# Performance work log

Hardware: AMD Instinct MI355X
Metric: run time of the kernel (lower is better)

The kernel has to match this reference:

```python
import jax, jax.numpy as jnp
import numpy as np

B, L, D, NH, NITEMS = 256, 200, 128, 2, 100000
HD = D // NH
LAMB = 0.6
NEG = -1e9

_PARAM_SHAPES = dict(
    item_emb=(NITEMS, D), pos_emb=(L, D),
    W_ei=(D, D), b_ei=(D,), W_eo=(D, D), b_eo=(D,), b_iah=(D,), b_oah=(D,),
    w_ih=(3 * D, 2 * D), b_ih=(3 * D,), w_hh=(3 * D, D), b_hh=(3 * D,),
    ln1_g=(D,), ln1_b=(D,),
    Wq=(D, D), bq=(D,), Wk=(D, D), bk=(D,), Wv=(D, D), bv=(D,), Wo=(D, D), bo=(D,),
    ln2_g=(D,), ln2_b=(D,), W1=(D, D), b1=(D,), W2=(D, D), b2=(D,),
    lnf_g=(D,), lnf_b=(D,),
)


def setup_inputs() -> dict:
    key = jax.random.key(0)
    ks = jax.random.split(key, len(_PARAM_SHAPES) + 2)
    stdv = 1.0 / np.sqrt(D)  # GCSAN._init_weights: uniform(-stdv, stdv) on ALL params
    p = {}
    for i, (name, shp) in enumerate(_PARAM_SHAPES.items()):
        p[name] = jax.random.uniform(ks[i], shp, jnp.float32, -stdv, stdv)
    lens = jax.random.randint(ks[-2], (B,), L // 4, L + 1)
    vals = jax.random.randint(ks[-1], (B, L), 1, NITEMS)
    # trailing zero padding, as the original break-on-zero loop assumes
    seqs = jnp.where(jnp.arange(L)[None, :] < lens[:, None], vals, 0).astype(jnp.int32)
    p['seqs'] = seqs
    p['lens'] = lens.astype(jnp.int32)
    return p


def _ln(x, g, b):
    mu = x.mean(-1, keepdims=True)
    var = ((x - mu) ** 2).mean(-1, keepdims=True)
    return (x - mu) / jnp.sqrt(var + 1e-5) * g + b


def _build_graph(seqs):
    # Vectorized replacement of _get_slice (per-row np.unique + adjacency build)
    def per_row(seq):
        s = jnp.sort(seq)
        first = jnp.concatenate([jnp.ones((1,), bool), s[1:] != s[:-1]])
        pos = jnp.cumsum(first) - 1  # compaction target of each first-occurrence
        items = jnp.zeros((L,), seq.dtype).at[jnp.where(first, pos, L)].set(s, mode='drop')
        n_u = first.sum()
        search = jnp.where(jnp.arange(L) < n_u, items, jnp.iinfo(jnp.int32).max)
        alias = jnp.searchsorted(search, seq).astype(jnp.int32)
        return items, alias
    items, alias = jax.vmap(per_row)(seqs)
    valid = seqs[:, 1:] > 0  # edge (i -> i+1) exists until first pad
    u = jnp.where(valid, alias[:, :-1], L)  # route masked edges to dummy row L
    v = jnp.where(valid, alias[:, 1:], L)
    bidx = jnp.arange(B)[:, None]
    uA = jnp.zeros((B, L + 1, L + 1), jnp.float32).at[bidx, u, v].set(1.0)[:, :L, :L]
    in_deg = jnp.maximum(uA.sum(1), 1.0)
    out_deg = jnp.maximum(uA.sum(2), 1.0)
    A_in = jnp.swapaxes(uA, 1, 2) / in_deg[:, :, None]   # A[i,j] = uA[j,i]/in_deg[i]
    A_out = uA / out_deg[:, :, None]                     # A[i,k] = uA[i,k]/out_deg[i]
    return alias, jnp.concatenate([A_in, A_out], axis=2), items  # A: [B, L, 2L]


def reference(item_emb, pos_emb, W_ei, b_ei, W_eo, b_eo, b_iah, b_oah,
              w_ih, b_ih, w_hh, b_hh, ln1_g, ln1_b, Wq, bq, Wk, bk, Wv, bv,
              Wo, bo, ln2_g, ln2_b, W1, b1, W2, b2, lnf_g, lnf_b, seqs, lens):
    alias, A, items = _build_graph(seqs)
    hidden = item_emb[items]  # [B, L, D]
    # SR-GNN gated cell, step = n_layers = 1
    for _ in range(1):
        h_in = jnp.einsum('bij,bjd->bid', A[:, :, :L], hidden @ W_ei.T + b_ei) + b_iah
        h_out = jnp.einsum('bij,bjd->bid', A[:, :, L:], hidden @ W_eo.T + b_eo) + b_oah
        gi = jnp.concatenate([h_in, h_out], -1) @ w_ih.T + b_ih
        gh = hidden @ w_hh.T + b_hh
        i_r, i_i, i_n = jnp.split(gi, 3, -1)
        h_r, h_i, h_n = jnp.split(gh, 3, -1)
        r = jax.nn.sigmoid(i_r + h_r)
        z = jax.nn.sigmoid(i_i + h_i)
        ng = jnp.tanh(i_n + r * h_n)
        hidden = ng + z * (hidden - ng)
    bidx = jnp.arange(B)
    seq_hidden = hidden[bidx[:, None], alias]  # alias-gather back to sequence order
    last_idx = lens - 1
    ht = seq_hidden[bidx, last_idx]
    x = seq_hidden + pos_emb[None, :, :]
    tl_mask = (seqs > 0)[:, :, None].astype(x.dtype)
    x = x * tl_mask
    causal = jnp.triu(jnp.ones((L, L), bool), 1)  # True = masked future (bidirectional=False)
    # SASRec-style block: ln -> MHA residual -> ln -> pointwise FFN residual
    q_in = _ln(x, ln1_g, ln1_b)
    heads = lambda t: t.reshape(B, L, NH, HD).transpose(0, 2, 1, 3)
    q = heads(q_in @ Wq.T + bq)
    k = heads(x @ Wk.T + bk)
    v = heads(x @ Wv.T + bv)
    sc = jnp.einsum('bhqd,bhkd->bhqk', q, k) / jnp.sqrt(jnp.asarray(HD, x.dtype))
    sc = jnp.where(causal[None, None], NEG, sc)
    attn = jax.nn.softmax(sc, -1)
    mo = jnp.einsum('bhqk,bhkd->bhqd', attn, v).transpose(0, 2, 1, 3).reshape(B, L, D) @ Wo.T + bo
    x = q_in + mo
    h = _ln(x, ln2_g, ln2_b)
    x = h + jax.nn.relu(h @ W1.T + b1) @ W2.T + b2
    x = x * tl_mask
    log_feats = _ln(x, lnf_g, lnf_b)
    out = log_feats[bidx, last_idx]
    return LAMB * out + (1.0 - LAMB) * ht
```

## Files before the change

kernel.cpp:

```cpp
#include <hip/hip_runtime.h>
#include <hip/hip_bf16.h>

#define Bb 256
#define Ll 200
#define Dd 128
#define BL (Bb*Ll)

typedef __hip_bfloat16 bf16;
typedef __attribute__((ext_vector_type(8))) short short8;
typedef __attribute__((ext_vector_type(4))) unsigned short ushort4v;
typedef __attribute__((ext_vector_type(4))) float floatx4;

__device__ __forceinline__ float b2f(bf16 v) { return __bfloat162float(v); }
__device__ __forceinline__ bf16  f2b(float v) { return __float2bfloat16(v); }
__device__ __forceinline__ float us2f(unsigned short u) { return __uint_as_float(((unsigned)u) << 16); }
__device__ __forceinline__ unsigned short f2us(float v) { bf16 t = f2b(v); return *(unsigned short*)&t; }
__device__ __forceinline__ float ldf(const void* p, int i, int f32) {
  return f32 ? ((const float*)p)[i] : b2f(((const bf16*)p)[i]);
}
__device__ __forceinline__ int detect_f32(const unsigned short* __restrict__ w) {
  unsigned short u = w[threadIdx.x & 63];
  return (__ballot(((u >> 7) & 0xFF) >= 0x7F) != 0ull) ? 1 : 0;
}
__device__ __forceinline__ void load_lds16(const void* g, void* l) {
  __builtin_amdgcn_global_load_lds((const __attribute__((address_space(1))) unsigned int*)g,
                                   (__attribute__((address_space(3))) unsigned int*)l, 16, 0, 0);
}

struct PackP {
  const void *W_ei,*W_eo,*w_ih,*w_hh,*Wk,*Wv,*Wqp,*Wop,*W1p,*W2p,*pos;
  const void *b_ei,*b_eo,*b_ih,*b_hh,*bk,*bv,*bqp,*bop,*b1p,*b2p,*biah,*boah;
  const void *ln1g,*ln1b,*ln2g,*ln2b,*lnfg,*lnfb;
  bf16 *cWhe,*cWih,*cWhh,*cWkv,*cWq,*cWo,*cW1,*cW2,*cPos;
  float *bias_he,*bias_gi,*bias_gh,*bias_kv,*cbq,*cbo,*cb1,*cb2,*cbiah,*cboah,*cln;
};
__global__ __launch_bounds__(256) void k0_pack(PackP p) {
  int idx = blockIdx.x * 256 + threadIdx.x;
  int f32 = detect_f32((const unsigned short*)p.W_ei);
  if (idx < 131072) {
    if (idx < 32768) {
      int r = idx >> 7, c = idx & 127;
      p.cWhe[idx] = f2b(r < 128 ? ldf(p.W_ei, r*128+c, f32) : ldf(p.W_eo, (r-128)*128+c, f32));
    } else p.cWih[idx-32768] = f2b(ldf(p.w_ih, idx-32768, f32));
  } else if (idx < 278528) {
    if (idx < 180224)      p.cWhh[idx-131072] = f2b(ldf(p.w_hh, idx-131072, f32));
    else if (idx < 212992) {
      int i = idx - 180224; int r = i >> 7, c = i & 127;
      p.cWkv[i] = f2b(r < 128 ? ldf(p.Wk, r*128+c, f32) : ldf(p.Wv, (r-128)*128+c, f32));
    }
    else if (idx < 229376) p.cWq[idx-212992] = f2b(ldf(p.Wqp, idx-212992, f32));
    else if (idx < 245760) p.cWo[idx-229376] = f2b(ldf(p.Wop, idx-229376, f32));
    else if (idx < 262144) p.cW1[idx-245760] = f2b(ldf(p.W1p, idx-245760, f32));
    else                   p.cW2[idx-262144] = f2b(ldf(p.W2p, idx-262144, f32));
  } else if (idx < 304128) {
    p.cPos[idx-278528] = f2b(ldf(p.pos, idx-278528, f32));
  } else {
    int j = idx - 304128;
    if      (j < 256)  p.bias_he[j]     = (j<128) ? ldf(p.b_ei,j,f32) : ldf(p.b_eo,j-128,f32);
    else if (j < 640)  p.bias_gi[j-256] = ldf(p.b_ih, j-256, f32);
    else if (j < 1024) p.bias_gh[j-640] = ldf(p.b_hh, j-640, f32);
    else if (j < 1280) { int c=j-1024; p.bias_kv[c] = (c<128)? ldf(p.bk,c,f32): ldf(p.bv,c-128,f32); }
    else if (j < 1408) p.cbq[j-1280]   = ldf(p.bqp, j-1280, f32);
    else if (j < 1536) p.cbo[j-1408]   = ldf(p.bop, j-1408, f32);
    else if (j < 1664) p.cb1[j-1536]   = ldf(p.b1p, j-1536, f32);
    else if (j < 1792) p.cb2[j-1664]   = ldf(p.b2p, j-1664, f32);
    else if (j < 1920) p.cbiah[j-1792] = ldf(p.biah, j-1792, f32);
    else if (j < 2048) p.cboah[j-1920] = ldf(p.boah, j-1920, f32);
    else {
      int i = j - 2048, g = i >> 7, c2 = i & 127;
      const void* s6 = g==0?p.ln1g: g==1?p.ln1b: g==2?p.ln2g: g==3?p.ln2b: g==4?p.lnfg: p.lnfb;
      p.cln[i] = ldf(s6, c2, f32);
    }
  }
}

__global__ __launch_bounds__(256) void k1_graph(const int* __restrict__ seqs,
    int* __restrict__ alias_g, int* __restrict__ items_g,
    float* __restrict__ rin_g, float* __restrict__ rout_g,
    unsigned* __restrict__ adj_g, unsigned* __restrict__ adjT_g)
{
  __shared__ int s[Ll], al[Ll], its[Ll];
  __shared__ unsigned char isf[Ll];
  __shared__ unsigned adjL[Ll*8], adjTL[Ll*8];
  int b = blockIdx.x, t = threadIdx.x;
  if (t < Ll) s[t] = seqs[b*Ll + t];
  for (int i = t; i < Ll*8; i += 256) { adjL[i] = 0u; adjTL[i] = 0u; }
  __syncthreads();
  if (t < Ll) {
    int v = s[t]; bool f = true;
    for (int j = 0; j < t; j++) if (s[j] == v) { f = false; break; }
    isf[t] = f ? 1 : 0; its[t] = 0;
  }
  __syncthreads();
  if (t < Ll) {
    int v = s[t], r = 0;
    for (int j = 0; j < Ll; j++) r += (isf[j] && s[j] < v);
    al[t] = r;
  }
  __syncthreads();
  if (t < Ll && isf[t]) its[al[t]] = s[t];
  if (t < Ll-1 && s[t+1] > 0) {
    int u = al[t], v = al[t+1];
    atomicOr(&adjL [u*8 + (v >> 5)], 1u << (v & 31));
    atomicOr(&adjTL[v*8 + (u >> 5)], 1u << (u & 31));
  }
  __syncthreads();
  if (t < Ll) {
    int od = 0, id = 0;
    for (int wd = 0; wd < 7; wd++) { od += __popc(adjL[t*8+wd]); id += __popc(adjTL[t*8+wd]); }
    rout_g [b*Ll + t] = 1.0f / (float)max(od, 1);
    rin_g  [b*Ll + t] = 1.0f / (float)max(id, 1);
    alias_g[b*Ll + t] = al[t];
    items_g[b*Ll + t] = its[t];
  }
  for (int i = t; i < Ll*8; i += 256) { adj_g[b*Ll*8 + i] = adjL[i]; adjT_g[b*Ll*8 + i] = adjTL[i]; }
}

__global__ __launch_bounds__(256) void k2_gather(const void* __restrict__ emb, const void* __restrict__ wei,
    const int* __restrict__ items_g, bf16* __restrict__ hidden)
{
  int idx = blockIdx.x * 256 + threadIdx.x;
  int f32 = detect_f32((const unsigned short*)wei);
  int n = idx >> 4, jv = idx & 15;
  int it = items_g[n];
  short8 o;
  if (f32) {
    const float* e = (const float*)emb + (size_t)it * 128 + jv * 8;
#pragma unroll
    for (int j = 0; j < 8; j++) o[j] = (short)f2us(e[j]);
  } else {
    o = ((const short8*)((const bf16*)emb + (size_t)it * 128))[jv];
  }
  ((short8*)hidden)[idx] = o;
}

template<int K>
__global__ __launch_bounds__(256) void gemm5(const bf16* __restrict__ A, const bf16* __restrict__ W,
    const float* __restrict__ bias,
    bf16* __restrict__ out_lo, int Nlo, bf16* __restrict__ out_hi, int Nhi, int split)
{
  __shared__ short As[128*64];
  __shared__ short Ws[128*64];
  int t = threadIdx.x;
  int wave = t >> 6, lane = t & 63;
  int q = lane >> 4, mr = lane & 15;
  int wm = wave & 1, wn = wave >> 1;
  int m0 = blockIdx.x * 128, n0 = blockIdx.y * 128;
  int lr = lane >> 3, slot = lane & 7;
  int gch = slot ^ lr;
  floatx4 acc[4][4] = {};
  for (int k0 = 0; k0 < K; k0 += 64) {
#pragma unroll
    for (int i = 0; i < 4; i++) {
      int c = wave*4 + i;
      int r = c*8 + lr;
      load_lds16(A + (size_t)(m0 + r) * K + k0 + gch*8, &As[c*512]);
      load_lds16(W + (size_t)(n0 + r) * K + k0 + gch*8, &Ws[c*512]);
    }
    __syncthreads();
#pragma unroll
    for (int kk = 0; kk < 2; kk++) {
      short8 af[4], wf[4];
#pragma unroll
      for (int i = 0; i < 4; i++) {
        int row = wm*64 + i*16 + mr;
        af[i] = *(const short8*)(&As[row*64 + ((kk*4+q) ^ (mr&7))*8]);
      }
#pragma unroll
      for (int j = 0; j < 4; j++) {
        int row = wn*64 + j*16 + mr;
        wf[j] = *(const short8*)(&Ws[row*64 + ((kk*4+q) ^ (mr&7))*8]);
      }
#pragma unroll
      for (int i = 0; i < 4; i++)
#pragma unroll
        for (int j = 0; j < 4; j++)
          acc[i][j] = __builtin_amdgcn_mfma_f32_16x16x32_bf16(wf[j], af[i], acc[i][j], 0, 0, 0);
    }
    __syncthreads();
  }
#pragma unroll
  for (int j = 0; j < 4; j++) {
    int ng = n0 + wn*64 + j*16 + q*4;
    floatx4 bs = *(const floatx4*)(bias + ng);
    bf16* outp; int col, stride;
    if (ng < split) { outp = out_lo; col = ng; stride = Nlo; }
    else            { outp = out_hi; col = ng - split; stride = Nhi; }
#pragma unroll
    for (int i = 0; i < 4; i++) {
      int m = m0 + wm*64 + i*16 + mr;
      ushort4v o;
#pragma unroll
      for (int e = 0; e < 4; e++) o[e] = f2us(acc[i][j][e] + bs[e]);
      *(ushort4v*)(outp + (size_t)m * stride + col) = o;
    }
  }
}

__global__ __launch_bounds__(256) void k3_agg(const bf16* __restrict__ he,
    const unsigned* __restrict__ adj_g, const unsigned* __restrict__ adjT_g,
    const float* __restrict__ rin_g, const float* __restrict__ rout_g,
    const float* __restrict__ cbiah, const float* __restrict__ cboah, bf16* __restrict__ hio)
{
  int b = blockIdx.x / 25, chunk = blockIdx.x % 25;
  int wave = threadIdx.x >> 6, lane = threadIdx.x & 63;
  bool isIn = lane < 32;
  int c = isIn ? 4*lane : 128 + 4*(lane-32);
  const bf16* heb = he + (size_t)b * Ll * 256;
  bf16* hiob = hio + (size_t)b * Ll * 256;
  float bias0 = isIn ? cbiah[c]   : cboah[c-128];
  float bias1 = isIn ? cbiah[c+1] : cboah[c-127];
  float bias2 = isIn ? cbiah[c+2] : cboah[c-126];
  float bias3 = isIn ? cbiah[c+3] : cboah[c-125];
#pragma unroll
  for (int s = 0; s < 2; s++) {
    int i = chunk*8 + wave + 4*s;
    const unsigned* mrow = (isIn ? adjT_g : adj_g) + ((size_t)b*Ll + i) * 8;
    float a0=0.f, a1=0.f, a2=0.f, a3=0.f;
    for (int wd = 0; wd < 7; wd++) {
      unsigned bits = mrow[wd];
      while (bits) {
        int j = (wd << 5) + __builtin_ctz(bits); bits &= bits - 1;
        ushort4v h4 = *(const ushort4v*)(heb + (size_t)j*256 + c);
        a0 += us2f(h4.x); a1 += us2f(h4.y); a2 += us2f(h4.z); a3 += us2f(h4.w);
      }
    }
    float r = isIn ? rin_g[b*Ll + i] : rout_g[b*Ll + i];
    ushort4v o;
    o.x = f2us(bias0 + r*a0); o.y = f2us(bias1 + r*a1);
    o.z = f2us(bias2 + r*a2); o.w = f2us(bias3 + r*a3);
    *(ushort4v*)(hiob + (size_t)i*256 + c) = o;
  }
}

__global__ __launch_bounds__(256) void k4_gru(const bf16* __restrict__ gi, const bf16* __restrict__ gh,
                                              bf16* __restrict__ hidden)
{
  int idx = blockIdx.x * 256 + threadIdx.x;
  int n = idx >> 4, jv = idx & 15;
  const short8* gin = (const short8*)(gi + (size_t)n * 384);
  const short8* ghn = (const short8*)(gh + (size_t)n * 384);
  short8 vir = gin[jv], vii = gin[16+jv], vnn = gin[32+jv];
  short8 whr = ghn[jv], whi = ghn[16+jv], whn = ghn[32+jv];
  short8 hv  = ((const short8*)hidden)[idx];
  short8 o;
#pragma unroll
  for (int e = 0; e < 8; e++) {
    float ir = us2f((unsigned short)vir[e]), ii = us2f((unsigned short)vii[e]), inn = us2f((unsigned short)vnn[e]);
    float hr = us2f((unsigned short)whr[e]), hi = us2f((unsigned short)whi[e]), hn = us2f((unsigned short)whn[e]);
    float r  = 1.f / (1.f + __expf(-(ir + hr)));
    float z  = 1.f / (1.f + __expf(-(ii + hi)));
    float arg = inn + r * hn;
    float ex = __expf(-2.f * arg);
    float ng = (1.f - ex) / (1.f + ex);
    float h  = us2f((unsigned short)hv[e]);
    o[e] = (short)f2us(ng + z * (h - ng));
  }
  ((short8*)hidden)[idx] = o;
}

__global__ __launch_bounds__(256) void k5_x(const bf16* __restrict__ hidden, const int* __restrict__ alias_g,
    const int* __restrict__ seqs, const int* __restrict__ lens,
    const bf16* __restrict__ cPos, bf16* __restrict__ x, float* __restrict__ ht)
{
  int idx = blockIdx.x * 256 + threadIdx.x;
  int jv = idx & 15; int bt = idx >> 4; int tpos = bt % Ll; int b = bt / Ll;
  int a = alias_g[bt];
  short8 hv = ((const short8*)(hidden + ((size_t)b*Ll + a) * Dd))[jv];
  short8 pv = ((const short8*)(cPos + tpos * Dd))[jv];
  bool valid = seqs[bt] > 0;
  bool isLast = (tpos == lens[b] - 1);
  short8 o;
#pragma unroll
  for (int e = 0; e < 8; e++) {
    float sh = us2f((unsigned short)hv[e]);
    float val = valid ? sh + us2f((unsigned short)pv[e]) : 0.f;
    o[e] = (short)f2us(val);
    if (isLast) ht[b*Dd + jv*8 + e] = sh;
  }
  ((short8*)x)[idx] = o;
}

struct FinalP {
  const bf16 *x, *kv; const float* ht;
  const bf16 *cWq, *cWo, *cW1, *cW2;
  const float *cbq, *cbo, *cb1, *cb2, *cln;
  const int* lens; const void* wei;
  void* out;
};
__device__ float block_sum(float v, float* red) {
  int t = threadIdx.x;
  red[t] = v; __syncthreads();
  for (int s = 128; s > 0; s >>= 1) { if (t < s) red[t] += red[t+s]; __syncthreads(); }
  float r = red[0]; __syncthreads(); return r;
}
__device__ float block_max(float v, float* red) {
  int t = threadIdx.x;
  red[t] = v; __syncthreads();
  for (int s = 128; s > 0; s >>= 1) { if (t < s) red[t] = fmaxf(red[t], red[t+s]); __syncthreads(); }
  float r = red[0]; __syncthreads(); return r;
}
__device__ __forceinline__ float dot128(const bf16* __restrict__ wrow, const float* __restrict__ vin) {
  const short8* wr = (const short8*)wrow;
  float acc = 0.f;
#pragma unroll
  for (int kk = 0; kk < 16; kk++) {
    short8 w8 = wr[kk];
#pragma unroll
    for (int j = 0; j < 8; j++) acc += vin[kk*8 + j] * us2f((unsigned short)w8[j]);
  }
  return acc;
}
__global__ __launch_bounds__(256) void k7_final(FinalP p)
{
  __shared__ float red[256];
  __shared__ float pb[256];
  __shared__ float av4[256];
  __shared__ float qin[128], qv[128], aout[128], hh[128], f1[128];
  int b = blockIdx.x, t = threadIdx.x, c = t;
  int li = p.lens[b] - 1;
  int f32 = detect_f32((const unsigned short*)p.wei);
  float xv = (c < 128) ? b2f(p.x[((size_t)b*Ll + li) * Dd + c]) : 0.f;
  float mu = block_sum((c < 128) ? xv : 0.f, red) * (1.f/128.f);
  float d  = (c < 128) ? xv - mu : 0.f;
  float var = block_sum(d*d, red) * (1.f/128.f);
  float rs = rsqrtf(var + 1e-5f);
  if (c < 128) qin[c] = d * rs * p.cln[c] + p.cln[128+c];
  __syncthreads();
  if (c < 128) qv[c] = p.cbq[c] + dot128(p.cWq + c*128, qin);
  __syncthreads();
  const bf16* kvb = p.kv + (size_t)b * Ll * 256;
  for (int h = 0; h < 2; h++) {
    float sc = -3.0e38f;
    if (t <= li) {
      const short8* kr = (const short8*)(kvb + (size_t)t*256 + h*64);
      float s_ = 0.f;
#pragma unroll
      for (int kk = 0; kk < 8; kk++) {
        short8 k8 = kr[kk];
#pragma unroll
        for (int j = 0; j < 8; j++) s_ += qv[h*64 + kk*8 + j] * us2f((unsigned short)k8[j]);
      }
      sc = s_ * 0.125f;
    }
    float m = block_max(sc, red);
    float e = (t <= li) ? __expf(sc - m) : 0.f;
    pb[t] = e;
    float l = block_sum(e, red);
    int ch = t & 63, part = t >> 6;
    float accv = 0.f;
    for (int j = part; j <= li; j += 4)
      accv += pb[j] * b2f(kvb[(size_t)j*256 + 128 + h*64 + ch]);
    av4[part*64 + ch] = accv;
    __syncthreads();
    if (t < 64) aout[h*64 + t] = (av4[t] + av4[64+t] + av4[128+t] + av4[192+t]) / l;
    __syncthreads();
  }
  float x2v = 0.f;
  if (c < 128) x2v = qin[c] + p.cbo[c] + dot128(p.cWo + c*128, aout);
  mu = block_sum((c < 128) ? x2v : 0.f, red) * (1.f/128.f);
  d  = (c < 128) ? x2v - mu : 0.f;
  var = block_sum(d*d, red) * (1.f/128.f);
  rs = rsqrtf(var + 1e-5f);
  if (c < 128) hh[c] = d * rs * p.cln[256+c] + p.cln[384+c];
  __syncthreads();
  if (c < 128) f1[c] = fmaxf(p.cb1[c] + dot128(p.cW1 + c*128, hh), 0.f);
  __syncthreads();
  float x3v = 0.f;
  if (c < 128) x3v = hh[c] + p.cb2[c] + dot128(p.cW2 + c*128, f1);
  mu = block_sum((c < 128) ? x3v : 0.f, red) * (1.f/128.f);
  d  = (c < 128) ? x3v - mu : 0.f;
  var = block_sum(d*d, red) * (1.f/128.f);
  rs = rsqrtf(var + 1e-5f);
  if (c < 128) {
    float lf = d * rs * p.cln[512+c] + p.cln[640+c];
    float outv = 0.6f * lf + 0.4f * p.ht[b*Dd + c];
    if (f32) ((float*)p.out)[b*Dd + c] = outv;
    else     ((bf16*)p.out)[b*Dd + c]  = f2b(outv);
  }
}

extern "C" void kernel_launch(void* const* d_in, const int* in_sizes, int n_in,
                              void* d_out, int out_size, void* d_ws, size_t ws_size,
                              hipStream_t stream)
{
  (void)in_sizes; (void)n_in; (void)out_size; (void)ws_size;
  const void* item_emb = d_in[0];
  const int* seqs = (const int*)d_in[30];
  const int* lens = (const int*)d_in[31];

  char* wsp = (char*)d_ws;
  size_t o = 0;
  auto alloc = [&](size_t sz) { void* p = wsp + o; o += (sz + 255) & ~(size_t)255; return p; };
  int*      alias_g = (int*)alloc((size_t)BL*4);
  int*      items_g = (int*)alloc((size_t)BL*4);
  float*    rin_g   = (float*)alloc((size_t)BL*4);
  float*    rout_g  = (float*)alloc((size_t)BL*4);
  unsigned* adj_g   = (unsigned*)alloc((size_t)BL*8*4);
  unsigned* adjT_g  = (unsigned*)alloc((size_t)BL*8*4);
  float*    ht_g    = (float*)alloc((size_t)Bb*Dd*4);
  bf16*     cWhe    = (bf16*)alloc(32768*2);
  bf16*     cWhh    = (bf16*)alloc(49152*2);
  bf16*     cWih    = (bf16*)alloc(98304*2);
  bf16*     cWkv    = (bf16*)alloc(32768*2);
  bf16*     cWq     = (bf16*)alloc(16384*2);
  bf16*     cWo     = (bf16*)alloc(16384*2);
  bf16*     cW1     = (bf16*)alloc(16384*2);
  bf16*     cW2     = (bf16*)alloc(16384*2);
  bf16*     cPos    = (bf16*)alloc(25600*2);
  float*    bias_he = (float*)alloc(256*4);
  float*    bias_gh = (float*)alloc(384*4);
  float*    bias_gi = (float*)alloc(384*4);
  float*    bias_kv = (float*)alloc(256*4);
  float*    cbq     = (float*)alloc(128*4);
  float*    cbo     = (float*)alloc(128*4);
  float*    cb1     = (float*)alloc(128*4);
  float*    cb2     = (float*)alloc(128*4);
  float*    cbiah   = (float*)alloc(128*4);
  float*    cboah   = (float*)alloc(128*4);
  float*    cln     = (float*)alloc(768*4);
  bf16*     hidden  = (bf16*)alloc((size_t)BL*128*2);
  bf16*     he      = (bf16*)alloc((size_t)BL*256*2);
  bf16*     hio     = (bf16*)alloc((size_t)BL*256*2);
  bf16*     gi      = (bf16*)alloc((size_t)BL*384*2);
  bf16*     gh      = (bf16*)alloc((size_t)BL*384*2);
  bf16*     x  = he;
  bf16*     kv = hio;

  PackP pp = { d_in[2], d_in[4], d_in[8], d_in[10], d_in[16], d_in[18], d_in[14], d_in[20],
               d_in[24], d_in[26], d_in[1],
               d_in[3], d_in[5], d_in[9], d_in[11], d_in[17], d_in[19], d_in[15], d_in[21],
               d_in[25], d_in[27], d_in[6], d_in[7],
               d_in[12], d_in[13], d_in[22], d_in[23], d_in[28], d_in[29],
               cWhe, cWih, cWhh, cWkv, cWq, cWo, cW1, cW2, cPos,
               bias_he, bias_gi, bias_gh, bias_kv, cbq, cbo, cb1, cb2, cbiah, cboah, cln };
  k0_pack<<<1199, 256, 0, stream>>>(pp);
  k1_graph<<<Bb, 256, 0, stream>>>(seqs, alias_g, items_g, rin_g, rout_g, adj_g, adjT_g);
  k2_gather<<<BL*16/256, 256, 0, stream>>>(item_emb, d_in[2], items_g, hidden);
  gemm5<128><<<dim3(BL/128, 5), 256, 0, stream>>>(hidden, cWhe, bias_he, he, 256, gh, 384, 256);
  k3_agg<<<Bb*25, 256, 0, stream>>>(he, adj_g, adjT_g, rin_g, rout_g, cbiah, cboah, hio);
  gemm5<256><<<dim3(BL/128, 3), 256, 0, stream>>>(hio, cWih, bias_gi, gi, 384, gi, 384, 1<<30);
  k4_gru<<<BL*16/256, 256, 0, stream>>>(gi, gh, hidden);
  k5_x<<<BL*16/256, 256, 0, stream>>>(hidden, alias_g, seqs, lens, cPos, x, ht_g);
  gemm5<128><<<dim3(BL/128, 2), 256, 0, stream>>>(x, cWkv, bias_kv, kv, 256, kv, 256, 1<<30);
  FinalP fp = { x, kv, ht_g, cWq, cWo, cW1, cW2, cbq, cbo, cb1, cb2, cln, lens, d_in[2], d_out };
  k7_final<<<Bb, 256, 0, stream>>>(fp);
}
```

Measured before the change: 321.9 us.

## Use wave-shuffle reductions and process both heads jointly in final kernel

Replaces the shared-memory tree reductions in the final per-sequence kernel with 64-lane shuffle reductions plus a small cross-wave combine. It also computes LayerNorm statistics in a single pass from sum and sum of squares. Both attention heads' scores and softmax are computed together, and the PV accumulation is split into 8 contiguous chunks with 4-wide vector loads. Dot products use four independent accumulators. This removes many __syncthreads barriers and serial dependency chains; single-pass variance is slightly less numerically robust.

```diff
diff --git a/kernel.cpp b/kernel.cpp
--- a/kernel.cpp
+++ b/kernel.cpp
@@ -288,92 +288,133 @@
   const int* lens; const void* wei;
   void* out;
 };
-__device__ float block_sum(float v, float* red) {
-  int t = threadIdx.x;
-  red[t] = v; __syncthreads();
-  for (int s = 128; s > 0; s >>= 1) { if (t < s) red[t] += red[t+s]; __syncthreads(); }
-  float r = red[0]; __syncthreads(); return r;
-}
-__device__ float block_max(float v, float* red) {
-  int t = threadIdx.x;
-  red[t] = v; __syncthreads();
-  for (int s = 128; s > 0; s >>= 1) { if (t < s) red[t] = fmaxf(red[t], red[t+s]); __syncthreads(); }
-  float r = red[0]; __syncthreads(); return r;
-}
-__device__ __forceinline__ float dot128(const bf16* __restrict__ wrow, const float* __restrict__ vin) {
+__device__ __forceinline__ float dot128i(const bf16* __restrict__ wrow, const float* __restrict__ vin) {
   const short8* wr = (const short8*)wrow;
-  float acc = 0.f;
-#pragma unroll
-  for (int kk = 0; kk < 16; kk++) {
-    short8 w8 = wr[kk];
-#pragma unroll
-    for (int j = 0; j < 8; j++) acc += vin[kk*8 + j] * us2f((unsigned short)w8[j]);
-  }
-  return acc;
+  float a0=0.f, a1=0.f, a2=0.f, a3=0.f;
+#pragma unroll
+  for (int kk = 0; kk < 4; kk++) {
+    short8 w0 = wr[kk*4+0], w1 = wr[kk*4+1], w2 = wr[kk*4+2], w3 = wr[kk*4+3];
+#pragma unroll
+    for (int j = 0; j < 8; j++) {
+      a0 += vin[kk*32 +      j] * us2f((unsigned short)w0[j]);
+      a1 += vin[kk*32 + 8  + j] * us2f((unsigned short)w1[j]);
+      a2 += vin[kk*32 + 16 + j] * us2f((unsigned short)w2[j]);
+      a3 += vin[kk*32 + 24 + j] * us2f((unsigned short)w3[j]);
+    }
+  }
+  return (a0+a1)+(a2+a3);
+}
+__device__ __forceinline__ float wave_sum(float v) {
+#pragma unroll
+  for (int m = 1; m < 64; m <<= 1) v += __shfl_xor(v, m, 64);
+  return v;
+}
+__device__ __forceinline__ float wave_max(float v) {
+#pragma unroll
+  for (int m = 1; m < 64; m <<= 1) v = fmaxf(v, __shfl_xor(v, m, 64));
+  return v;
 }
 __global__ __launch_bounds__(256) void k7_final(FinalP p)
 {
-  __shared__ float red[256];
-  __shared__ float pb[256];
-  __shared__ float av4[256];
+  __shared__ float sred[8];
   __shared__ float qin[128], qv[128], aout[128], hh[128], f1[128];
+  __shared__ float pb0[256], pb1[256];
+  __shared__ floatx4 av4[8][32];
   int b = blockIdx.x, t = threadIdx.x, c = t;
+  int w = t >> 6, ln = t & 63;
   int li = p.lens[b] - 1;
   int f32 = detect_f32((const unsigned short*)p.wei);
   float xv = (c < 128) ? b2f(p.x[((size_t)b*Ll + li) * Dd + c]) : 0.f;
-  float mu = block_sum((c < 128) ? xv : 0.f, red) * (1.f/128.f);
-  float d  = (c < 128) ? xv - mu : 0.f;
-  float var = block_sum(d*d, red) * (1.f/128.f);
-  float rs = rsqrtf(var + 1e-5f);
-  if (c < 128) qin[c] = d * rs * p.cln[c] + p.cln[128+c];
-  __syncthreads();
-  if (c < 128) qv[c] = p.cbq[c] + dot128(p.cWq + c*128, qin);
+  float s = wave_sum(xv), s2 = wave_sum(xv*xv);
+  if (ln == 0) { sred[w] = s; sred[4+w] = s2; }
+  __syncthreads();
+  float mu = (sred[0]+sred[1]+sred[2]+sred[3]) * (1.f/128.f);
+  float ms = (sred[4]+sred[5]+sred[6]+sred[7]) * (1.f/128.f);
+  float rs = rsqrtf(fmaxf(ms - mu*mu, 0.f) + 1e-5f);
+  __syncthreads();
+  if (c < 128) qin[c] = (xv - mu) * rs * p.cln[c] + p.cln[128+c];
+  __syncthreads();
+  if (c < 128) qv[c] = p.cbq[c] + dot128i(p.cWq + c*128, qin);
   __syncthreads();
   const bf16* kvb = p.kv + (size_t)b * Ll * 256;
-  for (int h = 0; h < 2; h++) {
-    float sc = -3.0e38f;
-    if (t <= li) {
-      const short8* kr = (const short8*)(kvb + (size_t)t*256 + h*64);
-      float s_ = 0.f;
-#pragma unroll
-      for (int kk = 0; kk < 8; kk++) {
-        short8 k8 = kr[kk];
-#pragma unroll
-        for (int j = 0; j < 8; j++) s_ += qv[h*64 + kk*8 + j] * us2f((unsigned short)k8[j]);
+  float s0 = -3.0e38f, s1 = -3.0e38f;
+  if (t <= li) {
+    const short8* kr = (const short8*)(kvb + (size_t)t*256);
+    float a00=0.f,a01=0.f,a10=0.f,a11=0.f;
+#pragma unroll
+    for (int kk = 0; kk < 4; kk++) {
+      short8 k0 = kr[kk*2], k1 = kr[kk*2+1], k2 = kr[8+kk*2], k3 = kr[8+kk*2+1];
+#pragma unroll
+      for (int j = 0; j < 8; j++) {
+        a00 += qv[kk*16 + j]      * us2f((unsigned short)k0[j]);
+        a01 += qv[kk*16 + 8 + j]  * us2f((unsigned short)k1[j]);
+        a10 += qv[64 + kk*16 + j]     * us2f((unsigned short)k2[j]);
+        a11 += qv[64 + kk*16 + 8 + j] * us2f((unsigned short)k3[j]);
       }
-      sc = s_ * 0.125f;
-    }
-    float m = block_max(sc, red);
-    float e = (t <= li) ? __expf(sc - m) : 0.f;
-    pb[t] = e;
-    float l = block_sum(e, red);
-    int ch = t & 63, part = t >> 6;
-    float accv = 0.f;
-    for (int j = part; j <= li; j += 4)
-      accv += pb[j] * b2f(kvb[(size_t)j*256 + 128 + h*64 + ch]);
-    av4[part*64 + ch] = accv;
-    __syncthreads();
-    if (t < 64) aout[h*64 + t] = (av4[t] + av4[64+t] + av4[128+t] + av4[192+t]) / l;
-    __syncthreads();
-  }
+    }
+    s0 = (a00+a01) * 0.125f; s1 = (a10+a11) * 0.125f;
+  }
+  float m0 = wave_max(s0), m1 = wave_max(s1);
+  if (ln == 0) { sred[w] = m0; sred[4+w] = m1; }
+  __syncthreads();
+  m0 = fmaxf(fmaxf(sred[0],sred[1]), fmaxf(sred[2],sred[3]));
+  m1 = fmaxf(fmaxf(sred[4],sred[5]), fmaxf(sred[6],sred[7]));
+  __syncthreads();
+  float e0 = (t <= li) ? __expf(s0 - m0) : 0.f;
+  float e1 = (t <= li) ? __expf(s1 - m1) : 0.f;
+  pb0[t] = e0; pb1[t] = e1;
+  float l0 = wave_sum(e0), l1 = wave_sum(e1);
+  if (ln == 0) { sred[w] = l0; sred[4+w] = l1; }
+  __syncthreads();
+  l0 = sred[0]+sred[1]+sred[2]+sred[3];
+  l1 = sred[4]+sred[5]+sred[6]+sred[7];
+  {
+    int part = t >> 5, cq = t & 31, ch = cq * 4;
+    int cnt = li + 1, cpp = (cnt + 7) >> 3;
+    int j0 = part * cpp, j1 = min(j0 + cpp, cnt);
+    const float* pbh = (ch < 64) ? pb0 : pb1;
+    float a0=0.f,a1=0.f,a2=0.f,a3=0.f;
+#pragma unroll 4
+    for (int j = j0; j < j1; j++) {
+      ushort4v v4 = *(const ushort4v*)(kvb + (size_t)j*256 + 128 + ch);
+      float pw = pbh[j];
+      a0 += pw*us2f(v4.x); a1 += pw*us2f(v4.y); a2 += pw*us2f(v4.z); a3 += pw*us2f(v4.w);
+    }
+    floatx4 o = {a0,a1,a2,a3};
+    av4[part][cq] = o;
+  }
+  __syncthreads();
+  if (c < 128) {
+    float l = (c < 64) ? l0 : l1;
+    float acc = 0.f;
+#pragma unroll
+    for (int pp = 0; pp < 8; pp++) acc += ((const float*)&av4[pp][c>>2])[c&3];
+    aout[c] = acc / l;
+  }
+  __syncthreads();
   float x2v = 0.f;
-  if (c < 128) x2v = qin[c] + p.cbo[c] + dot128(p.cWo + c*128, aout);
-  mu = block_sum((c < 128) ? x2v : 0.f, red) * (1.f/128.f);
-  d  = (c < 128) ? x2v - mu : 0.f;
-  var = block_sum(d*d, red) * (1.f/128.f);
-  rs = rsqrtf(var + 1e-5f);
-  if (c < 128) hh[c] = d * rs * p.cln[256+c] + p.cln[384+c];
-  __syncthreads();
-  if (c < 128) f1[c] = fmaxf(p.cb1[c] + dot128(p.cW1 + c*128, hh), 0.f);
+  if (c < 128) x2v = qin[c] + p.cbo[c] + dot128i(p.cWo + c*128, aout);
+  s = wave_sum((c<128)?x2v:0.f); s2 = wave_sum((c<128)?x2v*x2v:0.f);
+  if (ln == 0) { sred[w] = s; sred[4+w] = s2; }
+  __syncthreads();
+  mu = (sred[0]+sred[1]+sred[2]+sred[3]) * (1.f/128.f);
+  ms = (sred[4]+sred[5]+sred[6]+sred[7]) * (1.f/128.f);
+  rs = rsqrtf(fmaxf(ms - mu*mu, 0.f) + 1e-5f);
+  __syncthreads();
+  if (c < 128) hh[c] = (x2v - mu) * rs * p.cln[256+c] + p.cln[384+c];
+  __syncthreads();
+  if (c < 128) f1[c] = fmaxf(p.cb1[c] + dot128i(p.cW1 + c*128, hh), 0.f);
   __syncthreads();
   float x3v = 0.f;
-  if (c < 128) x3v = hh[c] + p.cb2[c] + dot128(p.cW2 + c*128, f1);
-  mu = block_sum((c < 128) ? x3v : 0.f, red) * (1.f/128.f);
-  d  = (c < 128) ? x3v - mu : 0.f;
-  var = block_sum(d*d, red) * (1.f/128.f);
-  rs = rsqrtf(var + 1e-5f);
+  if (c < 128) x3v = hh[c] + p.cb2[c] + dot128i(p.cW2 + c*128, f1);
+  s = wave_sum((c<128)?x3v:0.f); s2 = wave_sum((c<128)?x3v*x3v:0.f);
+  if (ln == 0) { sred[w] = s; sred[4+w] = s2; }
+  __syncthreads();
+  mu = (sred[0]+sred[1]+sred[2]+sred[3]) * (1.f/128.f);
+  ms = (sred[4]+sred[5]+sred[6]+sred[7]) * (1.f/128.f);
+  rs = rsqrtf(fmaxf(ms - mu*mu, 0.f) + 1e-5f);
   if (c < 128) {
-    float lf = d * rs * p.cln[512+c] + p.cln[640+c];
+    float lf = (x3v - mu) * rs * p.cln[512+c] + p.cln[640+c];
     float outv = 0.6f * lf + 0.4f * p.ht[b*Dd + c];
     if (f32) ((float*)p.out)[b*Dd + c] = outv;
     else     ((bf16*)p.out)[b*Dd + c]  = f2b(outv);
```

After: 290.1 us. -9.9%, faster.
